# Performance work log

Hardware: AMD Instinct MI355X
Metric: run time of the kernel (lower is better)

The kernel has to match this reference:

```python
import jax, jax.numpy as jnp
import numpy as np

N_NODES = 50000


def _sage_mean(x, src, dst, Wl, bl, Wr, n_nodes):
    # PyG SAGEConv (aggr='mean', root_weight=True): lin_l(mean_j x_j) + lin_r(x_i)
    msgs = x[src]                                             # [E, F] gather
    agg = jax.ops.segment_sum(msgs, dst, num_segments=n_nodes)  # [N, F]
    cnt = jax.ops.segment_sum(jnp.ones((src.shape[0],), x.dtype), dst,
                              num_segments=n_nodes)           # [N]
    mean = agg / jnp.maximum(cnt, 1.0)[:, None]
    return mean @ Wl + bl + x @ Wr


def setup_inputs() -> dict:
    key = jax.random.key(0)
    ks = jax.random.split(key, 12)
    in_ft = 64
    o0, o1, o2 = 64, 128, 128
    d2 = o0 + o0          # conv2 in = 128
    d3 = o0 + o0 + o1     # conv3 in = 256
    E = 800000

    def lin(k, fi, fo):
        s = 1.0 / np.sqrt(fi)
        return jax.random.uniform(k, (fi, fo), jnp.float32, -s, s)

    x = jax.random.normal(ks[0], (N_NODES, in_ft), jnp.float32)
    edge_index = jax.random.randint(ks[1], (2, E), 0, N_NODES, jnp.int64)
    return {
        "x": x,
        "edge_index": edge_index,
        "Wp": lin(ks[2], in_ft, o0), "bp": jnp.zeros((o0,), jnp.float32),
        "Wl1": lin(ks[3], in_ft, o0), "bl1": jnp.zeros((o0,), jnp.float32),
        "Wr1": lin(ks[4], in_ft, o0),
        "Wl2": lin(ks[5], d2, o1), "bl2": jnp.zeros((o1,), jnp.float32),
        "Wr2": lin(ks[6], d2, o1),
        "Wl3": lin(ks[7], d3, o2), "bl3": jnp.zeros((o2,), jnp.float32),
        "Wr3": lin(ks[8], d3, o2),
    }


def reference(x, edge_index, Wp, bp, Wl1, bl1, Wr1, Wl2, bl2, Wr2, Wl3, bl3, Wr3):
    src, dst = edge_index[0], edge_index[1]
    act = jax.nn.relu
    x_p = act(x @ Wp + bp)                                        # [N, o0]
    h1 = act(_sage_mean(x, src, dst, Wl1, bl1, Wr1, N_NODES))      # [N, o0]
    in2 = jnp.concatenate([x_p, h1], axis=1)                      # [N, 2*o0]
    h2 = act(_sage_mean(in2, src, dst, Wl2, bl2, Wr2, N_NODES))    # [N, o1]
    in3 = jnp.concatenate([x_p, h1, h2], axis=1)                  # [N, 2*o0+o1]
    h3 = act(_sage_mean(in3, src, dst, Wl3, bl3, Wr3, N_NODES))    # [N, o2]
    return h3
```

## Files before the change

kernel.cpp:

```cpp
#include <hip/hip_runtime.h>

#define N_NODES 50000
#define ELLW 48

typedef unsigned int uint;
typedef unsigned short ushort;
typedef float floatx4 __attribute__((ext_vector_type(4)));
typedef short short8 __attribute__((ext_vector_type(8)));

__device__ inline ushort f2bf(float f) {
    uint u = __float_as_uint(f);
    return (ushort)((u + 0x7fffu + ((u >> 16) & 1u)) >> 16);
}
__device__ inline float bflo(uint u) { return __uint_as_float(u << 16); }
__device__ inline float bfhi(uint u) { return __uint_as_float(u & 0xffff0000u); }


__device__ inline void swz_body(const float* __restrict__ W, ushort* __restrict__ Wz,
                                int O, int t) {
    int lane = t & 63, cb = t >> 6;
    int NBm = O / 16;
    int c = cb / NBm, nb = cb % NBm;
    int quad = lane >> 4, l16 = lane & 15;
#pragma unroll
    for (int j = 0; j < 8; j++) {
        float v = W[(size_t)(c * 32 + quad * 8 + j) * O + nb * 16 + l16];
        Wz[(size_t)t * 8 + j] = f2bf(v);
    }
}

__device__ void gemm1_body(int gb, const float* __restrict__ x,
                           const float* __restrict__ Wp, const float* __restrict__ bp,
                           ushort* __restrict__ feats, ushort* ldsA) {
    constexpr int LDA = 40;
    const int tid = threadIdx.x;
    const int wave = tid >> 6, lane = tid & 63;
    const int quad = lane >> 4, l16 = lane & 15;
    const int node0 = gb * 64;

    floatx4 acc[4];
#pragma unroll
    for (int nb = 0; nb < 4; nb++) acc[nb] = (floatx4){0.f, 0.f, 0.f, 0.f};

#pragma unroll
    for (int kk = 0; kk < 2; kk++) {
        const int k0 = kk * 32;
        __syncthreads();
        {
            int row = tid >> 2, seg = tid & 3;
            int node = node0 + row;
            float4 v0 = {0.f,0.f,0.f,0.f}, v1 = {0.f,0.f,0.f,0.f};
            if (node < N_NODES) {
                v0 = *(const float4*)&x[(size_t)node * 64 + k0 + seg * 8];
                v1 = *(const float4*)&x[(size_t)node * 64 + k0 + seg * 8 + 4];
            }
            ushort4 o0, o1;
            o0.x = f2bf(v0.x); o0.y = f2bf(v0.y); o0.z = f2bf(v0.z); o0.w = f2bf(v0.w);
            o1.x = f2bf(v1.x); o1.y = f2bf(v1.y); o1.z = f2bf(v1.z); o1.w = f2bf(v1.w);
            *(ushort4*)&ldsA[row * LDA + seg * 8] = o0;
            *(ushort4*)&ldsA[row * LDA + seg * 8 + 4] = o1;
        }
        __syncthreads();

        short8 a = *(const short8*)&ldsA[(wave * 16 + l16) * LDA + quad * 8];
#pragma unroll
        for (int nb = 0; nb < 4; nb++) {
            short8 bfrag;
#pragma unroll
            for (int j = 0; j < 8; j++)
                bfrag[j] = (short)f2bf(Wp[(size_t)(k0 + quad * 8 + j) * 64 + nb * 16 + l16]);
            acc[nb] = __builtin_amdgcn_mfma_f32_16x16x32_bf16(a, bfrag, acc[nb], 0, 0, 0);
        }
    }

#pragma unroll
    for (int nb = 0; nb < 4; nb++) {
        int ncol = nb * 16 + l16;
        float bv = bp[ncol];
#pragma unroll
        for (int r = 0; r < 4; r++) {
            int node = node0 + wave * 16 + quad * 4 + r;
            if (node >= N_NODES) continue;
            float v = fmaxf(acc[nb][r] + bv, 0.f);
            feats[(size_t)node * 256 + ncol] = f2bf(v);
        }
    }
}

__global__ __launch_bounds__(256) void k1_mega(
    const int* __restrict__ src, const int* __restrict__ dst, int E,
    int* __restrict__ fillc, ushort* __restrict__ ell,
    const float* __restrict__ x, ushort* __restrict__ xb,
    const float* __restrict__ Wp, const float* __restrict__ bp, ushort* __restrict__ feats,
    const float* __restrict__ Wl1, ushort* __restrict__ zl1,
    const float* __restrict__ Wr1, ushort* __restrict__ zr1,
    const float* __restrict__ Wl2, ushort* __restrict__ zl2,
    const float* __restrict__ Wr2, ushort* __restrict__ zr2,
    const float* __restrict__ Wl3, ushort* __restrict__ zl3,
    const float* __restrict__ Wr3, ushort* __restrict__ zr3,
    int NF, int NG, int NC)
{
    __shared__ ushort ldsA[64 * 40];
    int b = blockIdx.x, tid = threadIdx.x;
    if (b < NF) {
        int t = b * 256 + tid;
        if (t < E) {
            int d = dst[t], s = src[t];
            int p = atomicAdd(&fillc[d], 1);
            if (p < ELLW) ell[(size_t)d * ELLW + p] = (ushort)s;
        }
        return;
    }
    b -= NF;
    if (b < NG) { gemm1_body(b, x, Wp, bp, feats, ldsA); return; }
    b -= NG;
    if (b < NC) {
        int t = b * 256 + tid;
        float4 v = ((const float4*)x)[t];
        ushort4 o;
        o.x = f2bf(v.x); o.y = f2bf(v.y); o.z = f2bf(v.z); o.w = f2bf(v.w);
        ((ushort4*)xb)[t] = o;
        return;
    }
    b -= NC;
    if      (b < 2)  swz_body(Wl1, zl1, 64,  (b - 0) * 256 + tid);
    else if (b < 4)  swz_body(Wr1, zr1, 64,  (b - 2) * 256 + tid);
    else if (b < 12) swz_body(Wl2, zl2, 128, (b - 4) * 256 + tid);
    else if (b < 20) swz_body(Wr2, zr2, 128, (b - 12) * 256 + tid);
    else if (b < 36) swz_body(Wl3, zl3, 128, (b - 20) * 256 + tid);
    else             swz_body(Wr3, zr3, 128, (b - 36) * 256 + tid);
}


__global__ __launch_bounds__(256) void gather64_k(const int* __restrict__ fillc,
                                                  const ushort* __restrict__ ell,
                                                  const ushort* __restrict__ in, int sin,
                                                  ushort* __restrict__ out, int sout) {
    int node = blockIdx.x * 4 + (threadIdx.x >> 6);
    if (node >= N_NODES) return;
    int lane = threadIdx.x & 63;
    int half = lane >> 5, c = lane & 31;
    int n = fillc[node]; int nc = (n > ELLW) ? ELLW : n;
    const ushort* base = ell + (size_t)node * ELLW;
    float a0 = 0.f, a1 = 0.f;
    int i = half;
    for (; i + 2 < nc; i += 4) {
        int s0 = base[i], s1 = base[i + 2];
        uint u0 = *(const uint*)&in[(size_t)s0 * sin + 2 * c];
        uint u1 = *(const uint*)&in[(size_t)s1 * sin + 2 * c];
        a0 += bflo(u0) + bflo(u1);
        a1 += bfhi(u0) + bfhi(u1);
    }
    if (i < nc) {
        uint u0 = *(const uint*)&in[(size_t)base[i] * sin + 2 * c];
        a0 += bflo(u0);
        a1 += bfhi(u0);
    }
    a0 += __shfl_xor(a0, 32);
    a1 += __shfl_xor(a1, 32);
    if (half == 0) {
        float iv = 1.0f / fmaxf((float)n, 1.0f);
        uint r = (uint)f2bf(a0 * iv) | ((uint)f2bf(a1 * iv) << 16);
        *(uint*)&out[(size_t)node * sout + 2 * c] = r;
    }
}

__global__ __launch_bounds__(256) void gather128_k(const int* __restrict__ fillc,
                                                   const ushort* __restrict__ ell,
                                                   const ushort* __restrict__ in, int sin,
                                                   ushort* __restrict__ out, int sout) {
    int node = blockIdx.x * 4 + (threadIdx.x >> 6);
    if (node >= N_NODES) return;
    int lane = threadIdx.x & 63;
    int half = lane >> 5, c = lane & 31;
    int n = fillc[node]; int nc = (n > ELLW) ? ELLW : n;
    const ushort* base = ell + (size_t)node * ELLW;
    float a0 = 0.f, a1 = 0.f, a2 = 0.f, a3 = 0.f;
    int i = half;
    for (; i + 2 < nc; i += 4) {
        int s0 = base[i], s1 = base[i + 2];
        uint2 u0 = *(const uint2*)&in[(size_t)s0 * sin + 4 * c];
        uint2 u1 = *(const uint2*)&in[(size_t)s1 * sin + 4 * c];
        a0 += bflo(u0.x) + bflo(u1.x);
        a1 += bfhi(u0.x) + bfhi(u1.x);
        a2 += bflo(u0.y) + bflo(u1.y);
        a3 += bfhi(u0.y) + bfhi(u1.y);
    }
    if (i < nc) {
        uint2 u0 = *(const uint2*)&in[(size_t)base[i] * sin + 4 * c];
        a0 += bflo(u0.x); a1 += bfhi(u0.x);
        a2 += bflo(u0.y); a3 += bfhi(u0.y);
    }
    a0 += __shfl_xor(a0, 32);
    a1 += __shfl_xor(a1, 32);
    a2 += __shfl_xor(a2, 32);
    a3 += __shfl_xor(a3, 32);
    if (half == 0) {
        float iv = 1.0f / fmaxf((float)n, 1.0f);
        uint2 r;
        r.x = (uint)f2bf(a0 * iv) | ((uint)f2bf(a1 * iv) << 16);
        r.y = (uint)f2bf(a2 * iv) | ((uint)f2bf(a3 * iv) << 16);
        *(uint2*)&out[(size_t)node * sout + 4 * c] = r;
    }
}


template <int O, bool OUT_BF16>
__global__ __launch_bounds__(256) void mfma_gemm_k(
    const ushort* __restrict__ A1, int s1, int K1, const ushort* __restrict__ Wz1,
    const ushort* __restrict__ A2, int s2, int K2, const ushort* __restrict__ Wz2,
    const float* __restrict__ bias, void* __restrict__ outp, int so, int ocol)
{
    constexpr int NB = O / 16;
    constexpr int LDA = 40;
    __shared__ ushort ldsA[64 * LDA];

    const int tid = threadIdx.x;
    const int wave = tid >> 6, lane = tid & 63;
    const int quad = lane >> 4, l16 = lane & 15;
    const int node0 = blockIdx.x * 64;

    floatx4 acc[NB];
#pragma unroll
    for (int nb = 0; nb < NB; nb++) acc[nb] = (floatx4){0.f, 0.f, 0.f, 0.f};

#pragma unroll 1
    for (int phase = 0; phase < 2; ++phase) {
        const ushort* A = phase ? A2 : A1;
        const ushort* Wz = phase ? Wz2 : Wz1;
        const int K = phase ? K2 : K1;
        const int sA = phase ? s2 : s1;

#pragma unroll 1
        for (int k0 = 0; k0 < K; k0 += 32) {
            __syncthreads();
            {
                int row = tid >> 2, seg = tid & 3;
                int node = node0 + row;
                uint4 v = {0u, 0u, 0u, 0u};
                if (node < N_NODES)
                    v = *(const uint4*)&A[(size_t)node * sA + k0 + seg * 8];
                *(uint4*)&ldsA[row * LDA + seg * 8] = v;
            }
            __syncthreads();

            short8 a = *(const short8*)&ldsA[(wave * 16 + l16) * LDA + quad * 8];
            const short8* bz = (const short8*)Wz + (size_t)(k0 >> 5) * NB * 64;
#pragma unroll
            for (int nb = 0; nb < NB; nb++) {
                short8 b = bz[nb * 64 + lane];
                acc[nb] = __builtin_amdgcn_mfma_f32_16x16x32_bf16(a, b, acc[nb], 0, 0, 0);
            }
        }
    }

#pragma unroll
    for (int nb = 0; nb < NB; nb++) {
        int ncol = nb * 16 + l16;
        float bv = bias[ncol];
#pragma unroll
        for (int r = 0; r < 4; r++) {
            int node = node0 + wave * 16 + quad * 4 + r;
            if (node >= N_NODES) continue;
            float v = fmaxf(acc[nb][r] + bv, 0.f);
            if (OUT_BF16)
                ((ushort*)outp)[(size_t)node * so + ocol + ncol] = f2bf(v);
            else
                ((float*)outp)[(size_t)node * so + ocol + ncol] = v;
        }
    }
}


extern "C" void kernel_launch(void* const* d_in, const int* in_sizes, int n_in,
                              void* d_out, int out_size, void* d_ws, size_t ws_size,
                              hipStream_t stream) {
    const float* x   = (const float*)d_in[0];
    const int*   ei  = (const int*)d_in[1];
    const float* Wp  = (const float*)d_in[2];
    const float* bp  = (const float*)d_in[3];
    const float* Wl1 = (const float*)d_in[4];
    const float* bl1 = (const float*)d_in[5];
    const float* Wr1 = (const float*)d_in[6];
    const float* Wl2 = (const float*)d_in[7];
    const float* bl2 = (const float*)d_in[8];
    const float* Wr2 = (const float*)d_in[9];
    const float* Wl3 = (const float*)d_in[10];
    const float* bl3 = (const float*)d_in[11];
    const float* Wr3 = (const float*)d_in[12];

    const int E = in_sizes[1] / 2;
    const int N = N_NODES;
    const int* src = ei;
    const int* dst = ei + E;

    char* p = (char*)d_ws;
    ushort* xb    = (ushort*)p;  p += (size_t)N * 64 * 2;
    ushort* feats = (ushort*)p;  p += (size_t)N * 256 * 2;
    ushort* aggx  = (ushort*)p;  p += (size_t)N * 64 * 2;
    ushort* aggf  = (ushort*)p;  p += (size_t)N * 256 * 2;
    int* fillc    = (int*)p;     p += (size_t)N * 4;
    ushort* ell   = (ushort*)p;  p += (size_t)N * ELLW * 2;
    ushort* zl1   = (ushort*)p;  p += 64 * 64 * 2;
    ushort* zr1   = (ushort*)p;  p += 64 * 64 * 2;
    ushort* zl2   = (ushort*)p;  p += 128 * 128 * 2;
    ushort* zr2   = (ushort*)p;  p += 128 * 128 * 2;
    ushort* zl3   = (ushort*)p;  p += 256 * 128 * 2;
    ushort* zr3   = (ushort*)p;  p += 256 * 128 * 2;

    hipMemsetAsync(fillc, 0, (size_t)N * sizeof(int), stream);

    const int NF = (E + 255) / 256;
    const int NG = (N + 63) / 64;
    const int NC = (N * 64 / 4) / 256;

    k1_mega<<<NF + NG + NC + 52, 256, 0, stream>>>(
        src, dst, E, fillc, ell, x, xb, Wp, bp, feats,
        Wl1, zl1, Wr1, zr1, Wl2, zl2, Wr2, zr2, Wl3, zl3, Wr3, zr3,
        NF, NG, NC);

    gather64_k<<<(N + 3) / 4, 256, 0, stream>>>(fillc, ell, xb, 64, aggx, 64);

    mfma_gemm_k<64, true><<<NG, 256, 0, stream>>>(
        aggx, 64, 64, zl1, xb, 64, 64, zr1, bl1, feats, 256, 64);

    gather128_k<<<(N + 3) / 4, 256, 0, stream>>>(fillc, ell, feats, 256, aggf, 256);

    mfma_gemm_k<128, true><<<NG, 256, 0, stream>>>(
        aggf, 256, 128, zl2, feats, 256, 128, zr2, bl2, feats, 256, 128);

    gather128_k<<<(N + 3) / 4, 256, 0, stream>>>(fillc, ell, feats + 128, 256, aggf + 128, 256);

    mfma_gemm_k<128, false><<<NG, 256, 0, stream>>>(
        aggf, 256, 256, zl3, feats, 256, 256, zr3, bl3, (float*)d_out, 128, 0);
}
```

Before: 302.3 us.

## Fuse neighbor-mean gather with MFMA GEMM per SAGE layer

Replaces the separate gather and GEMM kernels with one fused kernel per layer. Each 64-node block computes the neighbor means into shared memory and then runs the MFMA products directly from there. This removes three launches and the global round trip of the aggregated features. Layer 2's aggregate is also written to a compact buffer so layer 3 can reuse it, and layer 3 only gathers the new h2 columns. The cost is lower parallelism during the gather: about 780 blocks instead of 12500, with each wave walking 16 nodes in series. Larger shared-memory use per block may also reduce occupancy for this latency-bound gather.

After: 375.2 us. 1.24x slower.

```diff
diff --git a/kernel.cpp b/kernel.cpp
--- a/kernel.cpp
+++ b/kernel.cpp
@@ -132,141 +132,289 @@
 }
 
 
-__global__ __launch_bounds__(256) void gather64_k(const int* __restrict__ fillc,
-                                                  const ushort* __restrict__ ell,
-                                                  const ushort* __restrict__ in, int sin,
-                                                  ushort* __restrict__ out, int sout) {
-    int node = blockIdx.x * 4 + (threadIdx.x >> 6);
-    if (node >= N_NODES) return;
-    int lane = threadIdx.x & 63;
-    int half = lane >> 5, c = lane & 31;
-    int n = fillc[node]; int nc = (n > ELLW) ? ELLW : n;
-    const ushort* base = ell + (size_t)node * ELLW;
-    float a0 = 0.f, a1 = 0.f;
-    int i = half;
-    for (; i + 2 < nc; i += 4) {
-        int s0 = base[i], s1 = base[i + 2];
-        uint u0 = *(const uint*)&in[(size_t)s0 * sin + 2 * c];
-        uint u1 = *(const uint*)&in[(size_t)s1 * sin + 2 * c];
-        a0 += bflo(u0) + bflo(u1);
-        a1 += bfhi(u0) + bfhi(u1);
-    }
-    if (i < nc) {
-        uint u0 = *(const uint*)&in[(size_t)base[i] * sin + 2 * c];
-        a0 += bflo(u0);
-        a1 += bfhi(u0);
-    }
-    a0 += __shfl_xor(a0, 32);
-    a1 += __shfl_xor(a1, 32);
-    if (half == 0) {
-        float iv = 1.0f / fmaxf((float)n, 1.0f);
-        uint r = (uint)f2bf(a0 * iv) | ((uint)f2bf(a1 * iv) << 16);
-        *(uint*)&out[(size_t)node * sout + 2 * c] = r;
-    }
-}
-
-__global__ __launch_bounds__(256) void gather128_k(const int* __restrict__ fillc,
-                                                   const ushort* __restrict__ ell,
-                                                   const ushort* __restrict__ in, int sin,
-                                                   ushort* __restrict__ out, int sout) {
-    int node = blockIdx.x * 4 + (threadIdx.x >> 6);
-    if (node >= N_NODES) return;
-    int lane = threadIdx.x & 63;
-    int half = lane >> 5, c = lane & 31;
-    int n = fillc[node]; int nc = (n > ELLW) ? ELLW : n;
-    const ushort* base = ell + (size_t)node * ELLW;
-    float a0 = 0.f, a1 = 0.f, a2 = 0.f, a3 = 0.f;
-    int i = half;
-    for (; i + 2 < nc; i += 4) {
-        int s0 = base[i], s1 = base[i + 2];
-        uint2 u0 = *(const uint2*)&in[(size_t)s0 * sin + 4 * c];
-        uint2 u1 = *(const uint2*)&in[(size_t)s1 * sin + 4 * c];
-        a0 += bflo(u0.x) + bflo(u1.x);
-        a1 += bfhi(u0.x) + bfhi(u1.x);
-        a2 += bflo(u0.y) + bflo(u1.y);
-        a3 += bfhi(u0.y) + bfhi(u1.y);
-    }
-    if (i < nc) {
-        uint2 u0 = *(const uint2*)&in[(size_t)base[i] * sin + 4 * c];
-        a0 += bflo(u0.x); a1 += bfhi(u0.x);
-        a2 += bflo(u0.y); a3 += bfhi(u0.y);
-    }
-    a0 += __shfl_xor(a0, 32);
-    a1 += __shfl_xor(a1, 32);
-    a2 += __shfl_xor(a2, 32);
-    a3 += __shfl_xor(a3, 32);
-    if (half == 0) {
-        float iv = 1.0f / fmaxf((float)n, 1.0f);
-        uint2 r;
-        r.x = (uint)f2bf(a0 * iv) | ((uint)f2bf(a1 * iv) << 16);
-        r.y = (uint)f2bf(a2 * iv) | ((uint)f2bf(a3 * iv) << 16);
-        *(uint2*)&out[(size_t)node * sout + 4 * c] = r;
-    }
-}
-
-
-template <int O, bool OUT_BF16>
-__global__ __launch_bounds__(256) void mfma_gemm_k(
-    const ushort* __restrict__ A1, int s1, int K1, const ushort* __restrict__ Wz1,
-    const ushort* __restrict__ A2, int s2, int K2, const ushort* __restrict__ Wz2,
-    const float* __restrict__ bias, void* __restrict__ outp, int so, int ocol)
+__global__ __launch_bounds__(256) void fused_h1_k(
+    const int* __restrict__ fillc, const ushort* __restrict__ ell,
+    const ushort* __restrict__ xb,
+    const ushort* __restrict__ zl1, const ushort* __restrict__ zr1,
+    const float* __restrict__ bl1, ushort* __restrict__ feats)
 {
-    constexpr int NB = O / 16;
-    constexpr int LDA = 40;
-    __shared__ ushort ldsA[64 * LDA];
-
+    constexpr int LDG = 72;
+    __shared__ ushort ldsG[64 * LDG];
+    __shared__ ushort ldsR[64 * LDG];
     const int tid = threadIdx.x;
     const int wave = tid >> 6, lane = tid & 63;
     const int quad = lane >> 4, l16 = lane & 15;
+    const int half = lane >> 5, c = lane & 31;
     const int node0 = blockIdx.x * 64;
 
-    floatx4 acc[NB];
-#pragma unroll
-    for (int nb = 0; nb < NB; nb++) acc[nb] = (floatx4){0.f, 0.f, 0.f, 0.f};
-
-#pragma unroll 1
-    for (int phase = 0; phase < 2; ++phase) {
-        const ushort* A = phase ? A2 : A1;
-        const ushort* Wz = phase ? Wz2 : Wz1;
-        const int K = phase ? K2 : K1;
-        const int sA = phase ? s2 : s1;
-
-#pragma unroll 1
-        for (int k0 = 0; k0 < K; k0 += 32) {
-            __syncthreads();
-            {
-                int row = tid >> 2, seg = tid & 3;
-                int node = node0 + row;
-                uint4 v = {0u, 0u, 0u, 0u};
-                if (node < N_NODES)
-                    v = *(const uint4*)&A[(size_t)node * sA + k0 + seg * 8];
-                *(uint4*)&ldsA[row * LDA + seg * 8] = v;
-            }
-            __syncthreads();
-
-            short8 a = *(const short8*)&ldsA[(wave * 16 + l16) * LDA + quad * 8];
-            const short8* bz = (const short8*)Wz + (size_t)(k0 >> 5) * NB * 64;
-#pragma unroll
-            for (int nb = 0; nb < NB; nb++) {
-                short8 b = bz[nb * 64 + lane];
-                acc[nb] = __builtin_amdgcn_mfma_f32_16x16x32_bf16(a, b, acc[nb], 0, 0, 0);
-            }
-        }
-    }
-
-#pragma unroll
-    for (int nb = 0; nb < NB; nb++) {
+#pragma unroll
+    for (int it = 0; it < 2; it++) {
+        int s = tid + it * 256;
+        int row = s >> 3, seg = s & 7;
+        int node = node0 + row;
+        uint4 v = {0u,0u,0u,0u};
+        if (node < N_NODES) v = *(const uint4*)&xb[(size_t)node * 64 + seg * 8];
+        *(uint4*)&ldsR[row * LDG + seg * 8] = v;
+    }
+
+    for (int mi = 0; mi < 16; mi++) {
+        int row = wave * 16 + mi;
+        int node = node0 + row;
+        if (node >= N_NODES) break;
+        int n = fillc[node]; int nc = (n > ELLW) ? ELLW : n;
+        const ushort* base = ell + (size_t)node * ELLW;
+        float a0 = 0.f, a1 = 0.f;
+        int i = half;
+        for (; i + 2 < nc; i += 4) {
+            int s0 = base[i], s1 = base[i + 2];
+            uint u0 = *(const uint*)&xb[(size_t)s0 * 64 + 2 * c];
+            uint u1 = *(const uint*)&xb[(size_t)s1 * 64 + 2 * c];
+            a0 += bflo(u0) + bflo(u1);
+            a1 += bfhi(u0) + bfhi(u1);
+        }
+        if (i < nc) {
+            uint u0 = *(const uint*)&xb[(size_t)base[i] * 64 + 2 * c];
+            a0 += bflo(u0); a1 += bfhi(u0);
+        }
+        a0 += __shfl_xor(a0, 32);
+        a1 += __shfl_xor(a1, 32);
+        if (half == 0) {
+            float iv = 1.0f / fmaxf((float)n, 1.0f);
+            *(uint*)&ldsG[row * LDG + 2 * c] = (uint)f2bf(a0 * iv) | ((uint)f2bf(a1 * iv) << 16);
+        }
+    }
+    __syncthreads();
+
+    floatx4 acc[4];
+#pragma unroll
+    for (int nb = 0; nb < 4; nb++) acc[nb] = (floatx4){0.f, 0.f, 0.f, 0.f};
+
+#pragma unroll
+    for (int kc = 0; kc < 2; kc++) {
+        short8 ag = *(const short8*)&ldsG[(wave * 16 + l16) * LDG + kc * 32 + quad * 8];
+        const short8* bzl = (const short8*)zl1 + (size_t)kc * 4 * 64;
+#pragma unroll
+        for (int nb = 0; nb < 4; nb++)
+            acc[nb] = __builtin_amdgcn_mfma_f32_16x16x32_bf16(ag, bzl[nb * 64 + lane], acc[nb], 0, 0, 0);
+        short8 ar = *(const short8*)&ldsR[(wave * 16 + l16) * LDG + kc * 32 + quad * 8];
+        const short8* bzr = (const short8*)zr1 + (size_t)kc * 4 * 64;
+#pragma unroll
+        for (int nb = 0; nb < 4; nb++)
+            acc[nb] = __builtin_amdgcn_mfma_f32_16x16x32_bf16(ar, bzr[nb * 64 + lane], acc[nb], 0, 0, 0);
+    }
+
+#pragma unroll
+    for (int nb = 0; nb < 4; nb++) {
         int ncol = nb * 16 + l16;
-        float bv = bias[ncol];
+        float bv = bl1[ncol];
 #pragma unroll
         for (int r = 0; r < 4; r++) {
             int node = node0 + wave * 16 + quad * 4 + r;
             if (node >= N_NODES) continue;
-            float v = fmaxf(acc[nb][r] + bv, 0.f);
-            if (OUT_BF16)
-                ((ushort*)outp)[(size_t)node * so + ocol + ncol] = f2bf(v);
-            else
-                ((float*)outp)[(size_t)node * so + ocol + ncol] = v;
+            feats[(size_t)node * 256 + 64 + ncol] = f2bf(fmaxf(acc[nb][r] + bv, 0.f));
+        }
+    }
+}
+
+__global__ __launch_bounds__(256) void fused_h2_k(
+    const int* __restrict__ fillc, const ushort* __restrict__ ell,
+    ushort* __restrict__ feats, ushort* __restrict__ aggA,
+    const ushort* __restrict__ zl2, const ushort* __restrict__ zr2,
+    const float* __restrict__ bl2)
+{
+    constexpr int LDG = 136;
+    __shared__ ushort ldsG[64 * LDG];
+    __shared__ ushort ldsR[64 * LDG];
+    const int tid = threadIdx.x;
+    const int wave = tid >> 6, lane = tid & 63;
+    const int quad = lane >> 4, l16 = lane & 15;
+    const int half = lane >> 5, c = lane & 31;
+    const int node0 = blockIdx.x * 64;
+
+#pragma unroll
+    for (int it = 0; it < 4; it++) {
+        int s = tid + it * 256;
+        int row = s >> 4, seg = s & 15;
+        int node = node0 + row;
+        uint4 v = {0u,0u,0u,0u};
+        if (node < N_NODES) v = *(const uint4*)&feats[(size_t)node * 256 + seg * 8];
+        *(uint4*)&ldsR[row * LDG + seg * 8] = v;
+    }
+
+    for (int mi = 0; mi < 16; mi++) {
+        int row = wave * 16 + mi;
+        int node = node0 + row;
+        if (node >= N_NODES) break;
+        int n = fillc[node]; int nc = (n > ELLW) ? ELLW : n;
+        const ushort* base = ell + (size_t)node * ELLW;
+        float a0 = 0.f, a1 = 0.f, a2 = 0.f, a3 = 0.f;
+        int i = half;
+        for (; i + 2 < nc; i += 4) {
+            int s0 = base[i], s1 = base[i + 2];
+            uint2 u0 = *(const uint2*)&feats[(size_t)s0 * 256 + 4 * c];
+            uint2 u1 = *(const uint2*)&feats[(size_t)s1 * 256 + 4 * c];
+            a0 += bflo(u0.x) + bflo(u1.x);
+            a1 += bfhi(u0.x) + bfhi(u1.x);
+            a2 += bflo(u0.y) + bflo(u1.y);
+            a3 += bfhi(u0.y) + bfhi(u1.y);
+        }
+        if (i < nc) {
+            uint2 u0 = *(const uint2*)&feats[(size_t)base[i] * 256 + 4 * c];
+            a0 += bflo(u0.x); a1 += bfhi(u0.x);
+            a2 += bflo(u0.y); a3 += bfhi(u0.y);
+        }
+        a0 += __shfl_xor(a0, 32);
+        a1 += __shfl_xor(a1, 32);
+        a2 += __shfl_xor(a2, 32);
+        a3 += __shfl_xor(a3, 32);
+        if (half == 0) {
+            float iv = 1.0f / fmaxf((float)n, 1.0f);
+            uint2 r;
+            r.x = (uint)f2bf(a0 * iv) | ((uint)f2bf(a1 * iv) << 16);
+            r.y = (uint)f2bf(a2 * iv) | ((uint)f2bf(a3 * iv) << 16);
+            *(uint2*)&ldsG[row * LDG + 4 * c] = r;
+            *(uint2*)&aggA[(size_t)node * 128 + 4 * c] = r;
+        }
+    }
+    __syncthreads();
+
+    floatx4 acc[8];
+#pragma unroll
+    for (int nb = 0; nb < 8; nb++) acc[nb] = (floatx4){0.f, 0.f, 0.f, 0.f};
+
+#pragma unroll
+    for (int kc = 0; kc < 4; kc++) {
+        short8 ag = *(const short8*)&ldsG[(wave * 16 + l16) * LDG + kc * 32 + quad * 8];
+        const short8* bzl = (const short8*)zl2 + (size_t)kc * 8 * 64;
+#pragma unroll
+        for (int nb = 0; nb < 8; nb++)
+            acc[nb] = __builtin_amdgcn_mfma_f32_16x16x32_bf16(ag, bzl[nb * 64 + lane], acc[nb], 0, 0, 0);
+        short8 ar = *(const short8*)&ldsR[(wave * 16 + l16) * LDG + kc * 32 + quad * 8];
+        const short8* bzr = (const short8*)zr2 + (size_t)kc * 8 * 64;
+#pragma unroll
+        for (int nb = 0; nb < 8; nb++)
+            acc[nb] = __builtin_amdgcn_mfma_f32_16x16x32_bf16(ar, bzr[nb * 64 + lane], acc[nb], 0, 0, 0);
+    }
+
+#pragma unroll
+    for (int nb = 0; nb < 8; nb++) {
+        int ncol = nb * 16 + l16;
+        float bv = bl2[ncol];
+#pragma unroll
+        for (int r = 0; r < 4; r++) {
+            int node = node0 + wave * 16 + quad * 4 + r;
+            if (node >= N_NODES) continue;
+            feats[(size_t)node * 256 + 128 + ncol] = f2bf(fmaxf(acc[nb][r] + bv, 0.f));
+        }
+    }
+}
+
+__global__ __launch_bounds__(256) void fused_h3_k(
+    const int* __restrict__ fillc, const ushort* __restrict__ ell,
+    const ushort* __restrict__ feats, const ushort* __restrict__ aggA,
+    const ushort* __restrict__ zl3, const ushort* __restrict__ zr3,
+    const float* __restrict__ bl3, float* __restrict__ out)
+{
+    constexpr int LDG = 136, LDS_ = 40;
+    __shared__ ushort ldsG[64 * LDG];
+    __shared__ ushort stg[64 * LDS_];
+    const int tid = threadIdx.x;
+    const int wave = tid >> 6, lane = tid & 63;
+    const int quad = lane >> 4, l16 = lane & 15;
+    const int half = lane >> 5, c = lane & 31;
+    const int node0 = blockIdx.x * 64;
+
+    for (int mi = 0; mi < 16; mi++) {
+        int row = wave * 16 + mi;
+        int node = node0 + row;
+        if (node >= N_NODES) break;
+        int n = fillc[node]; int nc = (n > ELLW) ? ELLW : n;
+        const ushort* base = ell + (size_t)node * ELLW;
+        float a0 = 0.f, a1 = 0.f, a2 = 0.f, a3 = 0.f;
+        int i = half;
+        for (; i + 2 < nc; i += 4) {
+            int s0 = base[i], s1 = base[i + 2];
+            uint2 u0 = *(const uint2*)&feats[(size_t)s0 * 256 + 128 + 4 * c];
+            uint2 u1 = *(const uint2*)&feats[(size_t)s1 * 256 + 128 + 4 * c];
+            a0 += bflo(u0.x) + bflo(u1.x);
+            a1 += bfhi(u0.x) + bfhi(u1.x);
+            a2 += bflo(u0.y) + bflo(u1.y);
+            a3 += bfhi(u0.y) + bfhi(u1.y);
+        }
+        if (i < nc) {
+            uint2 u0 = *(const uint2*)&feats[(size_t)base[i] * 256 + 128 + 4 * c];
+            a0 += bflo(u0.x); a1 += bfhi(u0.x);
+            a2 += bflo(u0.y); a3 += bfhi(u0.y);
+        }
+        a0 += __shfl_xor(a0, 32);
+        a1 += __shfl_xor(a1, 32);
+        a2 += __shfl_xor(a2, 32);
+        a3 += __shfl_xor(a3, 32);
+        if (half == 0) {
+            float iv = 1.0f / fmaxf((float)n, 1.0f);
+            uint2 r;
+            r.x = (uint)f2bf(a0 * iv) | ((uint)f2bf(a1 * iv) << 16);
+            r.y = (uint)f2bf(a2 * iv) | ((uint)f2bf(a3 * iv) << 16);
+            *(uint2*)&ldsG[row * LDG + 4 * c] = r;
+        }
+    }
+
+    floatx4 acc[8];
+#pragma unroll
+    for (int nb = 0; nb < 8; nb++) acc[nb] = (floatx4){0.f, 0.f, 0.f, 0.f};
+
+#pragma unroll 1
+    for (int kc = 0; kc < 4; kc++) {
+        __syncthreads();
+        {
+            int row = tid >> 2, seg = tid & 3;
+            int node = node0 + row;
+            uint4 v = {0u,0u,0u,0u};
+            if (node < N_NODES) v = *(const uint4*)&aggA[(size_t)node * 128 + kc * 32 + seg * 8];
+            *(uint4*)&stg[row * LDS_ + seg * 8] = v;
+        }
+        __syncthreads();
+        short8 a = *(const short8*)&stg[(wave * 16 + l16) * LDS_ + quad * 8];
+        const short8* bz = (const short8*)zl3 + (size_t)kc * 8 * 64;
+#pragma unroll
+        for (int nb = 0; nb < 8; nb++)
+            acc[nb] = __builtin_amdgcn_mfma_f32_16x16x32_bf16(a, bz[nb * 64 + lane], acc[nb], 0, 0, 0);
+    }
+#pragma unroll
+    for (int kc = 0; kc < 4; kc++) {
+        short8 a = *(const short8*)&ldsG[(wave * 16 + l16) * LDG + kc * 32 + quad * 8];
+        const short8* bz = (const short8*)zl3 + (size_t)(4 + kc) * 8 * 64;
+#pragma unroll
+        for (int nb = 0; nb < 8; nb++)
+            acc[nb] = __builtin_amdgcn_mfma_f32_16x16x32_bf16(a, bz[nb * 64 + lane], acc[nb], 0, 0, 0);
+    }
+#pragma unroll 1
+    for (int kc = 0; kc < 8; kc++) {
+        __syncthreads();
+        {
+            int row = tid >> 2, seg = tid & 3;
+            int node = node0 + row;
+            uint4 v = {0u,0u,0u,0u};
+            if (node < N_NODES) v = *(const uint4*)&feats[(size_t)node * 256 + kc * 32 + seg * 8];
+            *(uint4*)&stg[row * LDS_ + seg * 8] = v;
+        }
+        __syncthreads();
+        short8 a = *(const short8*)&stg[(wave * 16 + l16) * LDS_ + quad * 8];
+        const short8* bz = (const short8*)zr3 + (size_t)kc * 8 * 64;
+#pragma unroll
+        for (int nb = 0; nb < 8; nb++)
+            acc[nb] = __builtin_amdgcn_mfma_f32_16x16x32_bf16(a, bz[nb * 64 + lane], acc[nb], 0, 0, 0);
+    }
+
+#pragma unroll
+    for (int nb = 0; nb < 8; nb++) {
+        int ncol = nb * 16 + l16;
+        float bv = bl3[ncol];
+#pragma unroll
+        for (int r = 0; r < 4; r++) {
+            int node = node0 + wave * 16 + quad * 4 + r;
+            if (node >= N_NODES) continue;
+            out[(size_t)node * 128 + ncol] = fmaxf(acc[nb][r] + bv, 0.f);
         }
     }
 }
@@ -297,8 +445,7 @@
     char* p = (char*)d_ws;
     ushort* xb    = (ushort*)p;  p += (size_t)N * 64 * 2;
     ushort* feats = (ushort*)p;  p += (size_t)N * 256 * 2;
-    ushort* aggx  = (ushort*)p;  p += (size_t)N * 64 * 2;
-    ushort* aggf  = (ushort*)p;  p += (size_t)N * 256 * 2;
+    ushort* aggA  = (ushort*)p;  p += (size_t)N * 128 * 2;
     int* fillc    = (int*)p;     p += (size_t)N * 4;
     ushort* ell   = (ushort*)p;  p += (size_t)N * ELLW * 2;
     ushort* zl1   = (ushort*)p;  p += 64 * 64 * 2;
@@ -319,18 +466,9 @@
         Wl1, zl1, Wr1, zr1, Wl2, zl2, Wr2, zr2, Wl3, zl3, Wr3, zr3,
         NF, NG, NC);
 
-    gather64_k<<<(N + 3) / 4, 256, 0, stream>>>(fillc, ell, xb, 64, aggx, 64);
-
-    mfma_gemm_k<64, true><<<NG, 256, 0, stream>>>(
-        aggx, 64, 64, zl1, xb, 64, 64, zr1, bl1, feats, 256, 64);
-
-    gather128_k<<<(N + 3) / 4, 256, 0, stream>>>(fillc, ell, feats, 256, aggf, 256);
-
-    mfma_gemm_k<128, true><<<NG, 256, 0, stream>>>(
-        aggf, 256, 128, zl2, feats, 256, 128, zr2, bl2, feats, 256, 128);
-
-    gather128_k<<<(N + 3) / 4, 256, 0, stream>>>(fillc, ell, feats + 128, 256, aggf + 128, 256);
-
-    mfma_gemm_k<128, false><<<NG, 256, 0, stream>>>(
-        aggf, 256, 256, zl3, feats, 256, 256, zr3, bl3, (float*)d_out, 128, 0);
-}
+    fused_h1_k<<<NG, 256, 0, stream>>>(fillc, ell, xb, zl1, zr1, bl1, feats);
+
+    fused_h2_k<<<NG, 256, 0, stream>>>(fillc, ell, feats, aggA, zl2, zr2, bl2);
+
+    fused_h3_k<<<NG, 256, 0, stream>>>(fillc, ell, feats, aggA, zl3, zr3, bl3, (float*)d_out);
+}
```
